# Kernel tuning notes

Measured on AMD Instinct MI355X. Metric: run time of the kernel, lower is better.

## Reference

```python
import jax, jax.numpy as jnp
import numpy as np

DIM = 1024
SEQ_LEN = 4096
K_RANK = 256
HEADS = 16
HEAD_DIM = DIM // HEADS
BATCH = 4


def setup_inputs() -> dict:
    key = jax.random.key(0)
    k1, k2, k3, k4 = jax.random.split(key, 4)
    x = jax.random.normal(k1, (BATCH, SEQ_LEN, DIM), dtype=jnp.float32)
    W_qkv = jax.random.normal(k2, (DIM, 3 * DIM), dtype=jnp.float32) * (DIM ** -0.5)
    E = jax.random.normal(k3, (SEQ_LEN, K_RANK), dtype=jnp.float32)
    W_out = jax.random.normal(k4, (DIM, DIM), dtype=jnp.float32) * (DIM ** -0.5)
    b_out = jnp.zeros((DIM,), dtype=jnp.float32)
    return {"x": x, "W_qkv": W_qkv, "E": E, "W_out": W_out, "b_out": b_out}


def reference(x, W_qkv, E, W_out, b_out):
    B, N, D = x.shape
    scale = HEAD_DIM ** -0.5
    qkv = x @ W_qkv                                    # [B, N, 3D]
    q, k, v = jnp.split(qkv, 3, axis=-1)
    # [B, N, D] -> [B, H, N, hd]
    reshape_heads = lambda t: t.reshape(B, N, HEADS, HEAD_DIM).transpose(0, 2, 1, 3)
    q, k, v = map(reshape_heads, (q, k, v))
    # Linformer low-rank projection along sequence: [B, H, N, hd] -> [B, H, k, hd]
    k_proj = jnp.einsum('bhnd,nk->bhkd', k, E)
    v_proj = jnp.einsum('bhnd,nk->bhkd', v, E)
    scores = jnp.einsum('bhnd,bhkd->bhnk', q, k_proj) * scale  # [B, H, N, k]
    attn = jax.nn.softmax(scores, axis=-1)
    out = jnp.einsum('bhnk,bhkd->bhnd', attn, v_proj)  # [B, H, N, hd]
    out = out.transpose(0, 2, 1, 3).reshape(B, N, D)
    return out @ W_out + b_out
```

## Files before the change

kernel.cpp:

```cpp
#include <hip/hip_runtime.h>
#include <hip/hip_bf16.h>

typedef _Float16 f16;
typedef __attribute__((ext_vector_type(4))) _Float16 f16x4;
typedef __attribute__((ext_vector_type(8))) _Float16 f16x8;
typedef __attribute__((ext_vector_type(4))) float f32x4;

#define DIM 1024
#define SEQ 4096
#define KRNK 256
#define NH 16
#define HD 64
#define NB 4
#define ROWS (NB*SEQ)
#define NSPLIT 4

typedef const void __attribute__((address_space(1))) as1cv;
typedef void __attribute__((address_space(3))) as3v;

static __device__ __forceinline__ void glds16(const void* g, void* l) {
  __builtin_amdgcn_global_load_lds((as1cv*)g, (as3v*)l, 16, 0, 0);
}

template<int MODE>
__global__ __launch_bounds__(256) void k_prep_w(const float* __restrict__ in,
                                                f16* __restrict__ oh, f16* __restrict__ ol,
                                                int R, int C) {
  __shared__ float tile[64][65];
  int rtiles = R >> 6;
  int rt = blockIdx.x % rtiles, ct = blockIdx.x / rtiles;
  int r0 = rt << 6, c0 = ct << 6, t = threadIdx.x;
#pragma unroll
  for (int i = 0; i < 16; ++i) {
    int e = t + i * 256; int r = e >> 6, c = e & 63;
    tile[r][c] = in[(size_t)(r0 + r) * C + c0 + c];
  }
  __syncthreads();
#pragma unroll
  for (int i = 0; i < 16; ++i) {
    int e = t + i * 256; int c = e >> 6, r = e & 63;
    float v = tile[r][c];
    size_t idx = (size_t)(c0 + c) * R + r0 + r;
    if constexpr (MODE == 0) {
      v *= 256.0f;
      f16 h = (f16)v;
      oh[idx] = h;
      ol[idx] = (f16)(v - (float)h);
    } else {
      oh[idx] = (f16)v;
    }
  }
}

template<bool WH>
__global__ __launch_bounds__(256) void k_tsplit(const float* __restrict__ in,
                                                f16* __restrict__ oh,
                                                f16* __restrict__ oth,
                                                int R, int C) {
  __shared__ __align__(16) f16 tileT[64][66];
  int rtiles = R >> 6;
  int rt = blockIdx.x % rtiles, ct = blockIdx.x / rtiles;
  int r0 = rt << 6, c0 = ct << 6, t = threadIdx.x;
  int cq = (t & 15) * 4, rr = t >> 4;
#pragma unroll
  for (int i = 0; i < 4; ++i) {
    int r = rr + i * 16;
    f32x4 v = *(const f32x4*)&in[(size_t)(r0 + r) * C + c0 + cq];
    f16x4 h4 = {(f16)v[0], (f16)v[1], (f16)v[2], (f16)v[3]};
    if constexpr (WH) *(f16x4*)&oh[(size_t)(r0 + r) * C + c0 + cq] = h4;
#pragma unroll
    for (int k = 0; k < 4; ++k) tileT[cq + k][r] = h4[k];
  }
  __syncthreads();
  {
    int c = t >> 2, seg = t & 3;
    f16x8 a = *(const f16x8*)&tileT[c][seg * 16];
    f16x8 b = *(const f16x8*)&tileT[c][seg * 16 + 8];
    f16* dst = &oth[(size_t)(c0 + c) * R + r0 + seg * 16];
    *(f16x8*)dst = a;
    *(f16x8*)(dst + 8) = b;
  }
}

template<bool ASPL, bool BSPL, int MT, int NT>
static __device__ __forceinline__ void mm_core(
    const f16* __restrict__ Ah, const f16* __restrict__ Al, int lda,
    const f16* __restrict__ Bh, const f16* __restrict__ Bl, int ldb,
    int bm, int bn, int K,
    f16* sAh, f16* sAl, f16* sBh, f16* sBl,
    f32x4 (&acc)[MT / 32][NT / 32]) {
  constexpr int MREP = MT / 32, NREP = NT / 32;
  constexpr int AI = MT / 32, BI = NT / 32;
  const int t = threadIdx.x;
  const int lane = t & 63, w = t >> 6;
  const int wr = w >> 1, wc = w & 1;
  const int l15 = lane & 15, hi = lane >> 4;
  const f32x4 zero = {0.f, 0.f, 0.f, 0.f};
#pragma unroll
  for (int m = 0; m < MREP; ++m)
#pragma unroll
    for (int n = 0; n < NREP; ++n) acc[m][n] = zero;

  for (int kk = 0; kk < K; kk += 64) {
#pragma unroll
    for (int i = 0; i < AI; ++i) {
      int c = t + i * 256;
      int row = c >> 3, cc = c & 7;
      size_t g = (size_t)(bm + row) * lda + kk + ((cc ^ (row & 7)) * 8);
      glds16(Ah + g, &sAh[c * 8]);
      if constexpr (ASPL) glds16(Al + g, &sAl[c * 8]);
    }
#pragma unroll
    for (int i = 0; i < BI; ++i) {
      int c = t + i * 256;
      int row = c >> 3, cc = c & 7;
      size_t g = (size_t)(bn + row) * ldb + kk + ((cc ^ (row & 7)) * 8);
      glds16(Bh + g, &sBh[c * 8]);
      if constexpr (BSPL) glds16(Bl + g, &sBl[c * 8]);
    }
    __syncthreads();

    f16x8 avh[MREP][2], avl[MREP][2], bvh[NREP][2], bvl[NREP][2];
#pragma unroll
    for (int m = 0; m < MREP; ++m)
#pragma unroll
      for (int ks = 0; ks < 2; ++ks) {
        int R = wr * (MT / 2) + m * 16 + l15;
        int off = R * 64 + (((ks * 4 + hi) ^ (R & 7)) * 8);
        avh[m][ks] = *(const f16x8*)&sAh[off];
        if constexpr (ASPL) avl[m][ks] = *(const f16x8*)&sAl[off];
      }
#pragma unroll
    for (int n = 0; n < NREP; ++n)
#pragma unroll
      for (int ks = 0; ks < 2; ++ks) {
        int R = wc * (NT / 2) + n * 16 + l15;
        int off = R * 64 + (((ks * 4 + hi) ^ (R & 7)) * 8);
        bvh[n][ks] = *(const f16x8*)&sBh[off];
        if constexpr (BSPL) bvl[n][ks] = *(const f16x8*)&sBl[off];
      }
#pragma unroll
    for (int m = 0; m < MREP; ++m)
#pragma unroll
      for (int n = 0; n < NREP; ++n)
#pragma unroll
        for (int ks = 0; ks < 2; ++ks) {
          if constexpr (ASPL && BSPL) {
            acc[m][n] = __builtin_amdgcn_mfma_f32_16x16x32_f16(avl[m][ks], bvh[n][ks], acc[m][n], 0, 0, 0);
            acc[m][n] = __builtin_amdgcn_mfma_f32_16x16x32_f16(avh[m][ks], bvl[n][ks], acc[m][n], 0, 0, 0);
          } else if constexpr (BSPL) {
            acc[m][n] = __builtin_amdgcn_mfma_f32_16x16x32_f16(avh[m][ks], bvl[n][ks], acc[m][n], 0, 0, 0);
          }
          acc[m][n] = __builtin_amdgcn_mfma_f32_16x16x32_f16(avh[m][ks], bvh[n][ks], acc[m][n], 0, 0, 0);
        }
    __syncthreads();
  }
}

__global__ __launch_bounds__(256) void k_xe2(const f16* __restrict__ Eth,
                                             const f16* __restrict__ xth,
                                             float* __restrict__ XEp) {
  __shared__ __align__(16) f16 sA[128 * 64];
  __shared__ __align__(16) f16 sB[64 * 64];
  int bx = blockIdx.x;
  int nt = bx & 15, mt = (bx >> 4) & 1, b = (bx >> 5) & 3, sp = bx >> 7;
  int bm = mt << 7, bn = nt << 6;
  int koff = sp * (SEQ / NSPLIT);
  f32x4 acc[4][2];
  mm_core<false, false, 128, 64>(Eth + koff, nullptr, SEQ,
                                 xth + (size_t)b * SEQ + koff, nullptr, ROWS,
                                 bm, bn, SEQ / NSPLIT, sA, nullptr, sB, nullptr, acc);
  const int t = threadIdx.x, lane = t & 63, w = t >> 6;
  const int wr = w >> 1, wc = w & 1, l15 = lane & 15, hi = lane >> 4;
#pragma unroll
  for (int m = 0; m < 4; ++m)
#pragma unroll
    for (int n = 0; n < 2; ++n)
#pragma unroll
      for (int r = 0; r < 4; ++r) {
        int kr = bm + wr * 64 + m * 16 + hi * 4 + r;
        int dd = bn + wc * 32 + n * 16 + l15;
        XEp[(((size_t)sp * NB + b) * KRNK + kr) * DIM + dd] = acc[m][n][r];
      }
}

__global__ __launch_bounds__(256) void k_xered(const float* __restrict__ XEp,
                                               f16* __restrict__ XEh,
                                               f16* __restrict__ XEl) {
  size_t i = (size_t)blockIdx.x * 256 + threadIdx.x;
  const size_t sstride = (size_t)NB * KRNK * DIM / 4;
  const f32x4* p = (const f32x4*)XEp;
  f32x4 s = p[i];
#pragma unroll
  for (int sp = 1; sp < NSPLIT; ++sp) s += p[i + sp * sstride];
  f16x4 h4, l4;
#pragma unroll
  for (int j = 0; j < 4; ++j) {
    f16 h = (f16)s[j];
    h4[j] = h;
    l4[j] = (f16)(s[j] - (float)h);
  }
  *(f16x4*)&XEh[i * 4] = h4;
  *(f16x4*)&XEl[i * 4] = l4;
}

__global__ __launch_bounds__(256) void k_gq(const f16* __restrict__ xh,
                                            const f16* __restrict__ Wph,
                                            f16* __restrict__ q) {
  __shared__ __align__(16) f16 sA[64 * 64];
  __shared__ __align__(16) f16 sB[128 * 64];
  int bx = blockIdx.x;
  int mt = bx & 255, nt = bx >> 8;
  int bm = mt << 6, bn = nt << 7;
  f32x4 acc[2][4];
  mm_core<false, false, 64, 128>(xh, nullptr, DIM, Wph, nullptr, DIM, bm, bn, DIM,
                                 sA, nullptr, sB, nullptr, acc);
  const int t = threadIdx.x, lane = t & 63, w = t >> 6;
  const int wr = w >> 1, wc = w & 1, l15 = lane & 15, hi = lane >> 4;
#pragma unroll
  for (int m = 0; m < 2; ++m)
#pragma unroll
    for (int n = 0; n < 4; ++n)
#pragma unroll
      for (int r = 0; r < 4; ++r) {
        int row = bm + wr * 32 + m * 16 + hi * 4 + r;
        int col = bn + wc * 64 + n * 16 + l15;
        q[(size_t)row * DIM + col] = (f16)(acc[m][n][r] * (1.0f / 256.0f));
      }
}

__global__ __launch_bounds__(256) void k_t2(const f16* __restrict__ XEh,
                                            const f16* __restrict__ XEl,
                                            const f16* __restrict__ Wph,
                                            const f16* __restrict__ Wpl,
                                            f16* __restrict__ kph,
                                            f16* __restrict__ vpt) {
  __shared__ __align__(16) f16 sAh[128 * 64], sAl[128 * 64];
  __shared__ __align__(16) f16 sBh[64 * 64], sBl[64 * 64];
  int bx = blockIdx.x;
  int nt = bx & 15, mt = (bx >> 4) & 1, b = (bx >> 5) & 3, kv = bx >> 7;
  size_t abase = (size_t)b * KRNK * DIM;
  size_t wbase = (size_t)(DIM + kv * DIM) * DIM;
  f32x4 acc[4][2];
  mm_core<true, true, 128, 64>(XEh + abase, XEl + abase, DIM, Wph + wbase, Wpl + wbase, DIM,
                               mt << 7, nt << 6, DIM, sAh, sAl, sBh, sBl, acc);
  const int t = threadIdx.x, lane = t & 63, w = t >> 6;
  const int wr = w >> 1, wc = w & 1, l15 = lane & 15, hi = lane >> 4;
#pragma unroll
  for (int m = 0; m < 4; ++m)
#pragma unroll
    for (int n = 0; n < 2; ++n)
#pragma unroll
      for (int r = 0; r < 4; ++r) {
        int row = (mt << 7) + wr * 64 + m * 16 + hi * 4 + r;
        int col = (nt << 6) + wc * 32 + n * 16 + l15;
        float s = acc[m][n][r] * (1.0f / 256.0f);
        if (!kv) kph[((size_t)(b * KRNK + row)) * DIM + col] = (f16)s;
        else     vpt[((size_t)(b * DIM + col)) * KRNK + row] = (f16)s;
      }
}

__global__ __launch_bounds__(256) void k_attn(const f16* __restrict__ q,
                                              const f16* __restrict__ kph,
                                              const f16* __restrict__ vpt,
                                              f16* __restrict__ oattn) {
  __shared__ __align__(16) f16 sBuf[2][64 * 64];
  __shared__ __align__(16) f16 sP[64 * KRNK];
  int bx0 = blockIdx.x;
  int swz = (bx0 & 7) * 512 + (bx0 >> 3);
  int qb = swz & 63;
  int bh = swz >> 6;
  int b = bh >> 4, h = bh & 15;
  int t = threadIdx.x;
  int lane = t & 63, w = t >> 6;
  int l15 = lane & 15, hi = lane >> 4;

  const f16* kbase = kph + ((size_t)(b * KRNK)) * DIM + h * HD;
  const f16* vbase = vpt + ((size_t)(b * DIM + h * HD)) * KRNK;

  auto stageK = [&](int c, int bufi) {
#pragma unroll
    for (int i = 0; i < 2; ++i) {
      int sid = w * 128 + i * 64 + lane;
      int kr = sid >> 3, sl = sid & 7;
      glds16(kbase + (size_t)(c * 64 + kr) * DIM + ((sl ^ (kr & 7)) * 8),
             &sBuf[bufi][sid * 8]);
    }
  };
  auto stageV = [&](int c, int bufi) {
#pragma unroll
    for (int i = 0; i < 2; ++i) {
      int sid = w * 128 + i * 64 + lane;
      int hd = sid >> 3, sl = sid & 7;
      glds16(vbase + (size_t)hd * KRNK + c * 64 + ((sl ^ (hd & 7)) * 8),
             &sBuf[bufi][sid * 8]);
    }
  };

  int seqrow = qb * 64 + w * 16 + l15;
  const f16* qg = q + ((size_t)(b * SEQ + seqrow)) * DIM + h * HD;
  f16x8 aq[2];
  aq[0] = *(const f16x8*)(qg + hi * 8);
  aq[1] = *(const f16x8*)(qg + 32 + hi * 8);

  const f32x4 zero = {0.f, 0.f, 0.f, 0.f};
  f32x4 s[16];

  stageK(0, 0);
#pragma unroll
  for (int c = 0; c < 4; ++c) {
    __syncthreads();
    if (c < 3) stageK(c + 1, (c + 1) & 1);
    else       stageV(0, 0);
#pragma unroll
    for (int n = 0; n < 4; ++n) {
      int nn = c * 4 + n;
      s[nn] = zero;
      int krl = n * 16 + l15;
#pragma unroll
      for (int ks = 0; ks < 2; ++ks) {
        f16x8 bk = *(const f16x8*)&sBuf[c & 1][krl * 64 + (((ks * 4 + hi) ^ (krl & 7)) * 8)];
        s[nn] = __builtin_amdgcn_mfma_f32_16x16x32_f16(bk, aq[ks], s[nn], 0, 0, 0);
      }
    }
  }

  const float scale = 0.125f;
  float m0 = s[0][0];
#pragma unroll
  for (int n = 0; n < 16; ++n)
#pragma unroll
    for (int r = 0; r < 4; ++r) m0 = fmaxf(m0, s[n][r]);
  m0 = fmaxf(m0, __shfl_xor(m0, 16));
  m0 = fmaxf(m0, __shfl_xor(m0, 32));
  float sm0 = 0.f, sm1 = 0.f, sm2 = 0.f, sm3 = 0.f;
#pragma unroll
  for (int n = 0; n < 16; ++n) {
    float p0 = __expf((s[n][0] - m0) * scale);
    float p1 = __expf((s[n][1] - m0) * scale);
    float p2 = __expf((s[n][2] - m0) * scale);
    float p3 = __expf((s[n][3] - m0) * scale);
    s[n][0] = p0; s[n][1] = p1; s[n][2] = p2; s[n][3] = p3;
    sm0 += p0; sm1 += p1; sm2 += p2; sm3 += p3;
  }
  float sm = (sm0 + sm1) + (sm2 + sm3);
  sm += __shfl_xor(sm, 16);
  sm += __shfl_xor(sm, 32);
  float inv = 1.0f / sm;

  {
    int qrow = w * 16 + l15;
    int qm = qrow & 7;
    f16* rowp = &sP[qrow * KRNK];
#pragma unroll
    for (int n = 0; n < 16; ++n) {
      int chunk = 2 * n + (hi >> 1);
      f16x4 pv = {(f16)s[n][0], (f16)s[n][1], (f16)s[n][2], (f16)s[n][3]};
      *(f16x4*)&rowp[((chunk ^ qm) * 8) + (hi & 1) * 4] = pv;
    }
  }

  f32x4 o[4];
#pragma unroll
  for (int n = 0; n < 4; ++n) o[n] = zero;
  int qloc = w * 16 + l15;
#pragma unroll
  for (int c = 0; c < 4; ++c) {
    __syncthreads();
    if (c < 3) stageV(c + 1, (c + 1) & 1);
#pragma unroll
    for (int sub = 0; sub < 2; ++sub) {
      int chunk = c * 8 + sub * 4 + hi;
      f16x8 pa = *(const f16x8*)&sP[qloc * KRNK + ((chunk ^ (qloc & 7)) * 8)];
#pragma unroll
      for (int n = 0; n < 4; ++n) {
        int hd = n * 16 + l15;
        f16x8 bv = *(const f16x8*)&sBuf[c & 1][hd * 64 + (((sub * 4 + hi) ^ (hd & 7)) * 8)];
        o[n] = __builtin_amdgcn_mfma_f32_16x16x32_f16(pa, bv, o[n], 0, 0, 0);
      }
    }
  }

  float invr[4];
#pragma unroll
  for (int r = 0; r < 4; ++r) invr[r] = __shfl(inv, hi * 4 + r);

  size_t obase = ((size_t)(b * SEQ + qb * 64)) * DIM + h * HD;
#pragma unroll
  for (int n = 0; n < 4; ++n)
#pragma unroll
    for (int r = 0; r < 4; ++r) {
      int qloc2 = w * 16 + hi * 4 + r;
      int hd = n * 16 + l15;
      oattn[obase + (size_t)qloc2 * DIM + hd] = (f16)(o[n][r] * invr[r]);
    }
}

__global__ __launch_bounds__(256) void k_go(const f16* __restrict__ oattn,
                                            const f16* __restrict__ WoT,
                                            const float* __restrict__ bias,
                                            float* __restrict__ out) {
  __shared__ __align__(16) f16 sA[128 * 64];
  __shared__ __align__(16) f16 sB[128 * 64];
  int bx = blockIdx.x;
  int mt = bx & 127, nt = bx >> 7;
  int bm = mt << 7, bn = nt << 7;
  f32x4 acc[4][4];
  mm_core<false, false, 128, 128>(oattn, nullptr, DIM, WoT, nullptr, DIM, bm, bn, DIM,
                                  sA, nullptr, sB, nullptr, acc);
  const int t = threadIdx.x, lane = t & 63, w = t >> 6;
  const int wr = w >> 1, wc = w & 1, l15 = lane & 15, hi = lane >> 4;
#pragma unroll
  for (int m = 0; m < 4; ++m)
#pragma unroll
    for (int n = 0; n < 4; ++n)
#pragma unroll
      for (int r = 0; r < 4; ++r) {
        int row = bm + wr * 64 + m * 16 + hi * 4 + r;
        int col = bn + wc * 64 + n * 16 + l15;
        out[(size_t)row * DIM + col] = acc[m][n][r] + bias[col];
      }
}

extern "C" void kernel_launch(void* const* d_in, const int* in_sizes, int n_in,
                              void* d_out, int out_size, void* d_ws, size_t ws_size,
                              hipStream_t stream) {
  const float* x    = (const float*)d_in[0];
  const float* Wqkv = (const float*)d_in[1];
  const float* E    = (const float*)d_in[2];
  const float* Wout = (const float*)d_in[3];
  const float* bout = (const float*)d_in[4];
  float* out = (float*)d_out;

  char* p = (char*)d_ws;
  f16* Wph = (f16*)p;  p += (size_t)2 * 3 * DIM * DIM;
  f16* Wpl = (f16*)p;  p += (size_t)2 * 3 * DIM * DIM;
  f16* WoT = (f16*)p;  p += (size_t)2 * DIM * DIM;
  f16* xh  = (f16*)p;  p += (size_t)2 * ROWS * DIM;
  f16* xth = (f16*)p;  p += (size_t)2 * DIM * ROWS;
  f16* Eth = (f16*)p;  p += (size_t)2 * KRNK * SEQ;
  f16* XEh = (f16*)p;  p += (size_t)2 * NB * KRNK * DIM;
  f16* XEl = (f16*)p;  p += (size_t)2 * NB * KRNK * DIM;
  f16* kph = (f16*)p;  p += (size_t)2 * NB * KRNK * DIM;
  f16* vpt = (f16*)p;  p += (size_t)2 * NB * DIM * KRNK;
  f16* oattn = (f16*)p; p += (size_t)2 * ROWS * DIM;
  float* XEp = (float*)p;  p += (size_t)4 * NSPLIT * NB * KRNK * DIM;
  size_t need = (size_t)(p - (char*)d_ws);
  if (ws_size < need) return;

  f16* q = xth;

  k_prep_w<0><<<(DIM / 64) * (3 * DIM / 64), 256, 0, stream>>>(Wqkv, Wph, Wpl, DIM, 3 * DIM);
  k_prep_w<1><<<(DIM / 64) * (DIM / 64), 256, 0, stream>>>(Wout, WoT, nullptr, DIM, DIM);
  k_tsplit<true><<<(ROWS / 64) * (DIM / 64), 256, 0, stream>>>(x, xh, xth, ROWS, DIM);
  k_tsplit<false><<<(SEQ / 64) * (KRNK / 64), 256, 0, stream>>>(E, nullptr, Eth, SEQ, KRNK);
  k_xe2<<<512, 256, 0, stream>>>(Eth, xth, XEp);
  k_xered<<<(NB * KRNK * DIM / 4) / 256, 256, 0, stream>>>(XEp, XEh, XEl);
  k_gq<<<2048, 256, 0, stream>>>(xh, Wph, q);
  k_t2<<<256, 256, 0, stream>>>(XEh, XEl, Wph, Wpl, kph, vpt);
  k_attn<<<64 * 64, 256, 0, stream>>>(q, kph, vpt, oattn);
  k_go<<<1024, 256, 0, stream>>>(oattn, WoT, bout, out);
}
```

Baseline: 228.0 us.

## Merge weight-prep kernels, drop XE low-part split, widen attention K/V staging chunks

Fuses the two weight preparation launches into one kernel that branches on block index. Drops the low-order fp16 residual for the XE intermediate, so the K/V projection runs a single A operand instead of hi/lo, which saves a buffer, its writes and the extra MFMAs. In attention, K and V are staged in 128-row chunks with two iterations instead of four, halving barriers at the cost of doubled LDS buffers and lower occupancy. Dropping the XE residual reduces precision of the projected keys and values.

```diff
diff --git a/kernel.cpp b/kernel.cpp
--- a/kernel.cpp
+++ b/kernel.cpp
@@ -22,13 +22,19 @@
   __builtin_amdgcn_global_load_lds((as1cv*)g, (as3v*)l, 16, 0, 0);
 }
 
-template<int MODE>
-__global__ __launch_bounds__(256) void k_prep_w(const float* __restrict__ in,
-                                                f16* __restrict__ oh, f16* __restrict__ ol,
-                                                int R, int C) {
+__global__ __launch_bounds__(256) void k_prep_w_all(const float* __restrict__ Wqkv,
+                                                    const float* __restrict__ Wout,
+                                                    f16* __restrict__ Wph,
+                                                    f16* __restrict__ Wpl,
+                                                    f16* __restrict__ WoT) {
   __shared__ float tile[64][65];
+  int bx = blockIdx.x;
+  const float* in; f16* oh; f16* ol; int C; bool split;
+  if (bx < 768) { in = Wqkv; oh = Wph; ol = Wpl; C = 3 * DIM; split = true; }
+  else { bx -= 768; in = Wout; oh = WoT; ol = nullptr; C = DIM; split = false; }
+  const int R = DIM;
   int rtiles = R >> 6;
-  int rt = blockIdx.x % rtiles, ct = blockIdx.x / rtiles;
+  int rt = bx % rtiles, ct = bx / rtiles;
   int r0 = rt << 6, c0 = ct << 6, t = threadIdx.x;
 #pragma unroll
   for (int i = 0; i < 16; ++i) {
@@ -41,7 +47,7 @@
     int e = t + i * 256; int c = e >> 6, r = e & 63;
     float v = tile[r][c];
     size_t idx = (size_t)(c0 + c) * R + r0 + r;
-    if constexpr (MODE == 0) {
+    if (split) {
       v *= 256.0f;
       f16 h = (f16)v;
       oh[idx] = h;
@@ -185,23 +191,15 @@
 }
 
 __global__ __launch_bounds__(256) void k_xered(const float* __restrict__ XEp,
-                                               f16* __restrict__ XEh,
-                                               f16* __restrict__ XEl) {
+                                               f16* __restrict__ XEh) {
   size_t i = (size_t)blockIdx.x * 256 + threadIdx.x;
   const size_t sstride = (size_t)NB * KRNK * DIM / 4;
   const f32x4* p = (const f32x4*)XEp;
   f32x4 s = p[i];
 #pragma unroll
   for (int sp = 1; sp < NSPLIT; ++sp) s += p[i + sp * sstride];
-  f16x4 h4, l4;
-#pragma unroll
-  for (int j = 0; j < 4; ++j) {
-    f16 h = (f16)s[j];
-    h4[j] = h;
-    l4[j] = (f16)(s[j] - (float)h);
-  }
+  f16x4 h4 = {(f16)s[0], (f16)s[1], (f16)s[2], (f16)s[3]};
   *(f16x4*)&XEh[i * 4] = h4;
-  *(f16x4*)&XEl[i * 4] = l4;
 }
 
 __global__ __launch_bounds__(256) void k_gq(const f16* __restrict__ xh,
@@ -230,20 +228,19 @@
 }
 
 __global__ __launch_bounds__(256) void k_t2(const f16* __restrict__ XEh,
-                                            const f16* __restrict__ XEl,
                                             const f16* __restrict__ Wph,
                                             const f16* __restrict__ Wpl,
                                             f16* __restrict__ kph,
                                             f16* __restrict__ vpt) {
-  __shared__ __align__(16) f16 sAh[128 * 64], sAl[128 * 64];
+  __shared__ __align__(16) f16 sAh[128 * 64];
   __shared__ __align__(16) f16 sBh[64 * 64], sBl[64 * 64];
   int bx = blockIdx.x;
   int nt = bx & 15, mt = (bx >> 4) & 1, b = (bx >> 5) & 3, kv = bx >> 7;
   size_t abase = (size_t)b * KRNK * DIM;
   size_t wbase = (size_t)(DIM + kv * DIM) * DIM;
   f32x4 acc[4][2];
-  mm_core<true, true, 128, 64>(XEh + abase, XEl + abase, DIM, Wph + wbase, Wpl + wbase, DIM,
-                               mt << 7, nt << 6, DIM, sAh, sAl, sBh, sBl, acc);
+  mm_core<false, true, 128, 64>(XEh + abase, nullptr, DIM, Wph + wbase, Wpl + wbase, DIM,
+                                mt << 7, nt << 6, DIM, sAh, nullptr, sBh, sBl, acc);
   const int t = threadIdx.x, lane = t & 63, w = t >> 6;
   const int wr = w >> 1, wc = w & 1, l15 = lane & 15, hi = lane >> 4;
 #pragma unroll
@@ -264,7 +261,7 @@
                                               const f16* __restrict__ kph,
                                               const f16* __restrict__ vpt,
                                               f16* __restrict__ oattn) {
-  __shared__ __align__(16) f16 sBuf[2][64 * 64];
+  __shared__ __align__(16) f16 sBuf[2][128 * 64];
   __shared__ __align__(16) f16 sP[64 * KRNK];
   int bx0 = blockIdx.x;
   int swz = (bx0 & 7) * 512 + (bx0 >> 3);
@@ -280,20 +277,20 @@
 
   auto stageK = [&](int c, int bufi) {
 #pragma unroll
-    for (int i = 0; i < 2; ++i) {
-      int sid = w * 128 + i * 64 + lane;
-      int kr = sid >> 3, sl = sid & 7;
-      glds16(kbase + (size_t)(c * 64 + kr) * DIM + ((sl ^ (kr & 7)) * 8),
-             &sBuf[bufi][sid * 8]);
+    for (int i = 0; i < 4; ++i) {
+      int c2 = t + i * 256;
+      int kr = c2 >> 3, sl = c2 & 7;
+      glds16(kbase + (size_t)(c * 128 + kr) * DIM + ((sl ^ (kr & 7)) * 8),
+             &sBuf[bufi][c2 * 8]);
     }
   };
   auto stageV = [&](int c, int bufi) {
 #pragma unroll
-    for (int i = 0; i < 2; ++i) {
-      int sid = w * 128 + i * 64 + lane;
-      int hd = sid >> 3, sl = sid & 7;
-      glds16(vbase + (size_t)hd * KRNK + c * 64 + ((sl ^ (hd & 7)) * 8),
-             &sBuf[bufi][sid * 8]);
+    for (int i = 0; i < 4; ++i) {
+      int c2 = t + i * 256;
+      int hd = c2 >> 4, sl = c2 & 15;
+      glds16(vbase + (size_t)hd * KRNK + c * 128 + ((sl ^ (hd & 7)) * 8),
+             &sBuf[bufi][c2 * 8]);
     }
   };
 
@@ -308,18 +305,18 @@
 
   stageK(0, 0);
 #pragma unroll
-  for (int c = 0; c < 4; ++c) {
+  for (int c = 0; c < 2; ++c) {
     __syncthreads();
-    if (c < 3) stageK(c + 1, (c + 1) & 1);
-    else       stageV(0, 0);
-#pragma unroll
-    for (int n = 0; n < 4; ++n) {
-      int nn = c * 4 + n;
+    if (c == 0) stageK(1, 1);
+    else        stageV(0, 0);
+#pragma unroll
+    for (int n = 0; n < 8; ++n) {
+      int nn = c * 8 + n;
       s[nn] = zero;
       int krl = n * 16 + l15;
 #pragma unroll
       for (int ks = 0; ks < 2; ++ks) {
-        f16x8 bk = *(const f16x8*)&sBuf[c & 1][krl * 64 + (((ks * 4 + hi) ^ (krl & 7)) * 8)];
+        f16x8 bk = *(const f16x8*)&sBuf[c][krl * 64 + (((ks * 4 + hi) ^ (krl & 7)) * 8)];
         s[nn] = __builtin_amdgcn_mfma_f32_16x16x32_f16(bk, aq[ks], s[nn], 0, 0, 0);
       }
     }
@@ -365,17 +362,17 @@
   for (int n = 0; n < 4; ++n) o[n] = zero;
   int qloc = w * 16 + l15;
 #pragma unroll
-  for (int c = 0; c < 4; ++c) {
+  for (int c = 0; c < 2; ++c) {
     __syncthreads();
-    if (c < 3) stageV(c + 1, (c + 1) & 1);
-#pragma unroll
-    for (int sub = 0; sub < 2; ++sub) {
-      int chunk = c * 8 + sub * 4 + hi;
+    if (c == 0) stageV(1, 1);
+#pragma unroll
+    for (int q4 = 0; q4 < 4; ++q4) {
+      int chunk = c * 16 + q4 * 4 + hi;
       f16x8 pa = *(const f16x8*)&sP[qloc * KRNK + ((chunk ^ (qloc & 7)) * 8)];
 #pragma unroll
       for (int n = 0; n < 4; ++n) {
         int hd = n * 16 + l15;
-        f16x8 bv = *(const f16x8*)&sBuf[c & 1][hd * 64 + (((sub * 4 + hi) ^ (hd & 7)) * 8)];
+        f16x8 bv = *(const f16x8*)&sBuf[c][hd * 128 + (((q4 * 4 + hi) ^ (hd & 7)) * 8)];
         o[n] = __builtin_amdgcn_mfma_f32_16x16x32_f16(pa, bv, o[n], 0, 0, 0);
       }
     }
@@ -440,7 +437,6 @@
   f16* xth = (f16*)p;  p += (size_t)2 * DIM * ROWS;
   f16* Eth = (f16*)p;  p += (size_t)2 * KRNK * SEQ;
   f16* XEh = (f16*)p;  p += (size_t)2 * NB * KRNK * DIM;
-  f16* XEl = (f16*)p;  p += (size_t)2 * NB * KRNK * DIM;
   f16* kph = (f16*)p;  p += (size_t)2 * NB * KRNK * DIM;
   f16* vpt = (f16*)p;  p += (size_t)2 * NB * DIM * KRNK;
   f16* oattn = (f16*)p; p += (size_t)2 * ROWS * DIM;
@@ -450,14 +446,13 @@
 
   f16* q = xth;
 
-  k_prep_w<0><<<(DIM / 64) * (3 * DIM / 64), 256, 0, stream>>>(Wqkv, Wph, Wpl, DIM, 3 * DIM);
-  k_prep_w<1><<<(DIM / 64) * (DIM / 64), 256, 0, stream>>>(Wout, WoT, nullptr, DIM, DIM);
+  k_prep_w_all<<<1024, 256, 0, stream>>>(Wqkv, Wout, Wph, Wpl, WoT);
   k_tsplit<true><<<(ROWS / 64) * (DIM / 64), 256, 0, stream>>>(x, xh, xth, ROWS, DIM);
   k_tsplit<false><<<(SEQ / 64) * (KRNK / 64), 256, 0, stream>>>(E, nullptr, Eth, SEQ, KRNK);
   k_xe2<<<512, 256, 0, stream>>>(Eth, xth, XEp);
-  k_xered<<<(NB * KRNK * DIM / 4) / 256, 256, 0, stream>>>(XEp, XEh, XEl);
+  k_xered<<<(NB * KRNK * DIM / 4) / 256, 256, 0, stream>>>(XEp, XEh);
   k_gq<<<2048, 256, 0, stream>>>(xh, Wph, q);
-  k_t2<<<256, 256, 0, stream>>>(XEh, XEl, Wph, Wpl, kph, vpt);
+  k_t2<<<256, 256, 0, stream>>>(XEh, Wph, Wpl, kph, vpt);
   k_attn<<<64 * 64, 256, 0, stream>>>(q, kph, vpt, oattn);
   k_go<<<1024, 256, 0, stream>>>(oattn, WoT, bout, out);
 }
```

Result: no change. 225.8 us (-0.9%).
